# Kernel tuning notes

Measured on AMD Instinct MI355X. Metric: run time of the kernel, lower is better.

## Reference

```python
import jax, jax.numpy as jnp
import numpy as np

IMG_H = IMG_W = 640
NUM_CLASSES = 80
B = 8
NUM_ANCHORS = 76725
MAX_TOTAL = 200          # max_total_size == max_size_per_class
SCORE_TH = 0.5
IOU_TH = 0.5
K_CAND = 256             # per-class candidate pool for NMS (>= max survivors)
VARIANCES = jnp.asarray([0.1, 0.1, 0.2, 0.2], jnp.float32)


def _build_anchors(img_h, img_w):
    # RetinaNet AnchorBox: levels 3..7, 3 ratios x 3 scales, [cx, cy, w, h]
    ratios = [0.5, 1.0, 2.0]
    scales = [2.0 ** x for x in (0.0, 1.0 / 3.0, 2.0 / 3.0)]
    areas = [s * s for s in (32.0, 64.0, 128.0, 256.0, 512.0)]
    out = []
    for lvl, stride in enumerate([2 ** i for i in range(3, 8)]):
        dims = []
        for r in ratios:
            h = np.sqrt(areas[lvl] / r)
            w = areas[lvl] / h
            for s in scales:
                dims.append([w * s, h * s])
        dims = np.asarray(dims, np.float32)                      # [9,2]
        fh = int(np.ceil(img_h / stride)); fw = int(np.ceil(img_w / stride))
        rx = (np.arange(fw, dtype=np.float32) + 0.5) * stride
        ry = (np.arange(fh, dtype=np.float32) + 0.5) * stride
        cx, cy = np.meshgrid(rx, ry)
        centers = np.broadcast_to(np.stack([cx, cy], -1)[:, :, None, :], (fh, fw, 9, 2))
        d = np.broadcast_to(dims[None, None], (fh, fw, 9, 2))
        out.append(np.concatenate([centers, d], -1).reshape(-1, 4))
    return jnp.asarray(np.concatenate(out, 0))                   # [A,4]


def setup_inputs() -> dict:
    key = jax.random.key(0)
    k1, k2 = jax.random.split(key)
    box_pred = jax.random.normal(k1, (B, NUM_ANCHORS, 4), jnp.float32)
    cls_pred = jax.random.normal(k2, (B, NUM_ANCHORS, NUM_CLASSES), jnp.float32)
    anchor_boxes = _build_anchors(IMG_H, IMG_W)
    return {"box_pred": box_pred, "cls_pred": cls_pred, "anchor_boxes": anchor_boxes}


def _iou_one_vs_many(box, boxes):
    # box [4] vs boxes [K,4] in corner format
    lt = jnp.maximum(box[:2], boxes[:, :2])
    rb = jnp.minimum(box[2:], boxes[:, 2:])
    wh = jnp.maximum(rb - lt, 0.0)
    inter = wh[:, 0] * wh[:, 1]
    a1 = (box[2] - box[0]) * (box[3] - box[1])
    a2 = (boxes[:, 2] - boxes[:, 0]) * (boxes[:, 3] - boxes[:, 1])
    return inter / jnp.maximum(a1 + a2 - inter, 1e-8)


def _nms_keep(boxes, scores):
    # boxes [K,4] already sorted by descending score; greedy NMS
    eligible = scores > SCORE_TH
    idx = jnp.arange(K_CAND)

    def body(i, keep):
        iou = _iou_one_vs_many(boxes[i], boxes)
        suppress = (iou > IOU_TH) & (idx > i)
        return jnp.where(keep[i], keep & ~suppress, keep)

    keep = jax.lax.fori_loop(0, K_CAND, body, eligible)
    keep = keep & ((jnp.cumsum(keep) - 1) < MAX_TOTAL)           # max_size_per_class cap
    return keep


def _decode_and_nms(box_pred, cls_pred, anchor_boxes):
    scores_all = jax.nn.sigmoid(cls_pred)                        # [B,A,C]
    # decode: (dx,dy,dw,dh)*variances against [cx,cy,w,h] anchors
    d = box_pred * VARIANCES
    xy = d[..., :2] * anchor_boxes[None, :, 2:] + anchor_boxes[None, :, :2]
    wh = jnp.exp(d[..., 2:]) * anchor_boxes[None, :, 2:]
    boxes = jnp.concatenate([xy - 0.5 * wh, xy + 0.5 * wh], -1)  # [B,A,4] corners

    sc = jnp.swapaxes(scores_all, 1, 2)                          # [B,C,A]
    top_sc, top_idx = jax.lax.top_k(sc, K_CAND)                  # [B,C,K] sorted desc
    cand_boxes = jnp.take_along_axis(boxes[:, None], top_idx[..., None], axis=2)  # [B,C,K,4]

    keep = jax.lax.stop_gradient(jax.vmap(jax.vmap(_nms_keep))(cand_boxes, top_sc))  # [B,C,K]
    sel = jnp.where(keep, top_sc, -1.0)

    flat_sc = sel.reshape(B, -1)                                 # [B,C*K]
    flat_boxes = cand_boxes.reshape(B, -1, 4)
    flat_lbl = jnp.broadcast_to(jnp.arange(NUM_CLASSES)[None, :, None],
                                (B, NUM_CLASSES, K_CAND)).reshape(B, -1)

    fs, fi = jax.lax.top_k(flat_sc, MAX_TOTAL)                   # combine across classes
    out_boxes = jnp.take_along_axis(flat_boxes, fi[..., None], axis=1)
    out_lbl = jnp.take_along_axis(flat_lbl, fi, axis=1).astype(jnp.float32)
    valid = fs > 0.0                                             # pad invalid slots
    return (jnp.where(valid[..., None], out_boxes, 0.0),
            jnp.where(valid, fs, 0.0),
            jnp.where(valid, out_lbl, -1.0))


def reference(box_pred, cls_pred, anchor_boxes):
    return _decode_and_nms(box_pred, cls_pred, anchor_boxes)
```

## Files before the change

### kernel.cpp

```cpp
#include <hip/hip_runtime.h>
#include <math.h>
#include <stdint.h>

typedef unsigned long long u64;
typedef unsigned int u32;

#define NB 8
#define NA 76725
#define NC 80
#define KC 256
#define MAXT 200
#define CAP 2048
#define SELCAP 768
#define TAU 2.0f
#define CHUNK 512
#define NCHUNK 150
#define BCAP 48
#define CSTRIDE 16

#define OFF_BUFA      0ull
#define OFF_CLASSLIST 10485760ull
#define OFF_CANDBOX   11796480ull
#define OFF_COUNTS    14417920ull

__device__ __forceinline__ void kf_proc(float4 v, int i, int a0,
                                        u64 (*bucket)[BCAP], u32* bcnt) {
  int a = a0 + i / (NC / 4);
  int c0 = (i % (NC / 4)) * 4;
  float vv[4] = {v.x, v.y, v.z, v.w};
#pragma unroll
  for (int j = 0; j < 4; j++) {
    if (vv[j] > TAU) {
      int c = c0 + j;
      u32 pos = atomicAdd(&bcnt[c], 1u);
      if (pos < BCAP)
        bucket[c][pos] = ((u64)__float_as_uint(vv[j]) << 32) | (u32)a;
    }
  }
}

__global__ __launch_bounds__(256) void kfilter(const float* __restrict__ cls,
                                               u64* __restrict__ bufA,
                                               u32* __restrict__ counts) {
  __shared__ u64 bucket[NC][BCAP];
  __shared__ u32 bcnt[NC];
  __shared__ u32 gbase[NC];
  __shared__ u32 pref[NC + 1];

  const int b = blockIdx.x / NCHUNK;
  const int ch = blockIdx.x % NCHUNK;
  const int tid = threadIdx.x;
  const int a0 = ch * CHUNK;
  const int aN = (NA - a0) < CHUNK ? (NA - a0) : CHUNK;

  for (int i = tid; i < NC; i += 256) bcnt[i] = 0;
  __syncthreads();

  const float4* p = (const float4*)(cls + ((size_t)b * NA + a0) * NC);
  const int n4 = aN * (NC / 4);
  for (int i0 = tid; i0 < n4; i0 += 2048) {
    float4 v[8];
    bool g[8];
#pragma unroll
    for (int u = 0; u < 8; u++) {
      g[u] = (i0 + u * 256) < n4;
      if (g[u]) v[u] = p[i0 + u * 256];
    }
#pragma unroll
    for (int u = 0; u < 8; u++)
      if (g[u]) kf_proc(v[u], i0 + u * 256, a0, bucket, bcnt);
  }
  __syncthreads();
  if (tid < NC) {
    u32 n = bcnt[tid];
    if (n > BCAP) n = BCAP;
    bcnt[tid] = n;
    gbase[tid] = atomicAdd(&counts[(b * NC + tid) * CSTRIDE], n);
  }
  __syncthreads();
  if (tid == 0) {
    u32 s = 0;
    for (int c = 0; c < NC; c++) { pref[c] = s; s += bcnt[c]; }
    pref[NC] = s;
  }
  __syncthreads();
  const int total = (int)pref[NC];
  for (int e = tid; e < total; e += 256) {
    int lo = 0, hi = NC;
    while (lo + 1 < hi) { int mid = (lo + hi) >> 1; if ((int)pref[mid] <= e) lo = mid; else hi = mid; }
    int c = lo;
    int loc = e - (int)pref[c];
    u32 gb = gbase[c] + (u32)loc;
    if (gb < CAP)
      bufA[((size_t)(b * NC + c)) * CAP + gb] = bucket[c][loc];
  }
}

__global__ __launch_bounds__(256) void kselect(
    const float* __restrict__ cls, const float* __restrict__ boxp,
    const float* __restrict__ anc, u64* __restrict__ bufA,
    const u32* __restrict__ counts, u64* __restrict__ classList,
    float4* __restrict__ candBox) {
  __shared__ u64 sbuf[CAP];
  __shared__ u32 hist[1024];
  __shared__ u64 sel[SELCAP];
  __shared__ u64 skey[KC];
  __shared__ u64 scolT[4][KC];
  __shared__ float4 sBox[KC];
  __shared__ float sAr[KC];
  __shared__ int sNsel, sExtra, sSb;

  const int tid = threadIdx.x;
  const int bc = blockIdx.x;
  const int b = bc / NC, c = bc % NC;
  u64* buf = bufA + (size_t)bc * CAP;

  int cnt0 = (int)counts[bc * CSTRIDE];
  if (cnt0 > CAP) cnt0 = CAP;
  int cnt = cnt0;
  if (cnt0 < KC) {
    if (tid == 0) sExtra = 0;
    __syncthreads();
    for (int a = tid; a < NA; a += 256) {
      float x = cls[((size_t)b * NA + a) * NC + c];
      if (x > 0.0f && !(x > TAU)) {
        int pos = cnt0 + atomicAdd(&sExtra, 1);
        if (pos < CAP) buf[pos] = ((u64)__float_as_uint(x) << 32) | (u32)a;
      }
    }
    __syncthreads();
    cnt = cnt0 + sExtra;
  }
  if (cnt > CAP) cnt = CAP;

  for (int i = tid; i < 1024; i += 256) hist[i] = 0;
  if (tid == 0) sNsel = 0;
  skey[tid] = 0;
  for (int e = tid; e < cnt; e += 256) sbuf[e] = buf[e];
  __syncthreads();

  for (int e = tid; e < cnt; e += 256) {
    float f = __uint_as_float((u32)(sbuf[e] >> 32));
    int bin = (int)(f * 170.0f);
    bin = bin < 0 ? 0 : (bin > 1023 ? 1023 : bin);
    atomicAdd(&hist[bin], 1u);
  }
  __syncthreads();

  if (tid < 64) {
    int s = 0;
#pragma unroll
    for (int i = 0; i < 16; i++) s += (int)hist[tid * 16 + i];
    int suf = s;
#pragma unroll
    for (int d = 1; d < 64; d <<= 1) {
      int t = __shfl_down(suf, d, 64);
      if (tid + d < 64) suf += t;
    }
    u64 mask = __ballot(suf >= KC);
    int sb = mask ? (63 - __clzll((long long)mask)) : 0;
    if (tid == 0) sSb = sb;
  }
  __syncthreads();
  const int sb = sSb;

  for (int e = tid; e < cnt; e += 256) {
    u64 k = sbuf[e];
    float f = __uint_as_float((u32)(k >> 32));
    int bin = (int)(f * 170.0f);
    bin = bin < 0 ? 0 : (bin > 1023 ? 1023 : bin);
    if ((bin >> 4) >= sb) {
      float sc = 1.0f / (1.0f + expf(-f));
      u32 a = (u32)k;
      int pos = atomicAdd(&sNsel, 1);
      if (pos < SELCAP)
        sel[pos] = ((u64)__float_as_uint(sc) << 32) | (0xFFFFFFFFu - a);
    }
  }
  __syncthreads();
  int nsel = sNsel;
  if (nsel > SELCAP) nsel = SELCAP;

  for (int e = tid; e < nsel; e += 256) {
    u64 k = sel[e];
    int r = 0;
    for (int q = 0; q < nsel; q++) r += (sel[q] > k) ? 1 : 0;
    if (r < KC) skey[r] = k;
  }
  __syncthreads();

  {
    u64 k = skey[tid];
    u32 a = 0xFFFFFFFFu - (u32)k;
    if (k == 0ull || a >= NA) a = 0;
    float4 p = ((const float4*)boxp)[(size_t)b * NA + a];
    float4 an = ((const float4*)anc)[a];
    float dx = __fmul_rn(p.x, 0.1f), dy = __fmul_rn(p.y, 0.1f);
    float dw = __fmul_rn(p.z, 0.2f), dh = __fmul_rn(p.w, 0.2f);
    float cx = __fadd_rn(__fmul_rn(dx, an.z), an.x);
    float cy = __fadd_rn(__fmul_rn(dy, an.w), an.y);
    float w = __fmul_rn(expf(dw), an.z);
    float h = __fmul_rn(expf(dh), an.w);
    float4 bx;
    bx.x = __fsub_rn(cx, __fmul_rn(0.5f, w));
    bx.y = __fsub_rn(cy, __fmul_rn(0.5f, h));
    bx.z = __fadd_rn(cx, __fmul_rn(0.5f, w));
    bx.w = __fadd_rn(cy, __fmul_rn(0.5f, h));
    sBox[tid] = bx;
    sAr[tid] = __fmul_rn(__fsub_rn(bx.z, bx.x), __fsub_rn(bx.w, bx.y));
    candBox[(size_t)bc * KC + tid] = bx;
  }
  __syncthreads();

  {
    const int j = tid;
    float4 bj = sBox[j];
    float aj = sAr[j];
    u64 cw[4] = {0ull, 0ull, 0ull, 0ull};
    for (int i = 0; i < j; i++) {
      float4 bi = sBox[i];
      float ai = sAr[i];
      float lx = fmaxf(bi.x, bj.x), ly = fmaxf(bi.y, bj.y);
      float rx = fminf(bi.z, bj.z), ry = fminf(bi.w, bj.w);
      float wx = fmaxf(__fsub_rn(rx, lx), 0.0f);
      float wy = fmaxf(__fsub_rn(ry, ly), 0.0f);
      float inter = __fmul_rn(wx, wy);
      float uni = fmaxf(__fsub_rn(__fadd_rn(ai, aj), inter), 1e-8f);
      float iou = __fdiv_rn(inter, uni);
      if (iou > 0.5f) cw[i >> 6] |= (1ull << (i & 63));
    }
#pragma unroll
    for (int w = 0; w < 4; w++) scolT[w][j] = cw[w];
  }
  __syncthreads();

  if (tid < 64) {
    const int ln = tid;
    u64 C[4][4];
#pragma unroll
    for (int s = 0; s < 4; s++)
#pragma unroll
      for (int w = 0; w < 4; w++) C[s][w] = scolT[w][s * 64 + ln];
    int keep = 0;
#pragma unroll
    for (int s = 0; s < 4; s++)
      if (skey[s * 64 + ln] != 0ull) keep |= (1 << s);
#pragma unroll
    for (int w = 0; w < 4; w++) {
      u64 c0 = C[0][w], c1 = C[1][w], c2 = C[2][w], c3 = C[3][w];
      for (int t = 0; t < 64; t++) {
        int kt = __shfl(keep, t, 64);
        if ((kt >> w) & 1) {
          int sup = (int)((c0 >> t) & 1) | ((int)((c1 >> t) & 1) << 1) |
                    ((int)((c2 >> t) & 1) << 2) | ((int)((c3 >> t) & 1) << 3);
          keep &= ~sup;
        }
      }
    }
    u64 m[4];
#pragma unroll
    for (int s = 0; s < 4; s++) m[s] = __ballot((keep >> s) & 1);
    int tot = 0;
#pragma unroll
    for (int s = 0; s < 4; s++) tot += __popcll(m[s]);
    int keptTotal = tot < MAXT ? tot : MAXT;
    u64 lmask = (1ull << ln) - 1ull;
    int base = 0;
#pragma unroll
    for (int s = 0; s < 4; s++) {
      int j = s * 64 + ln;
      int cum = base + (int)__popcll(m[s] & lmask);
      if (((keep >> s) & 1) && cum < MAXT) {
        u64 hi = skey[j] >> 32;
        classList[(size_t)bc * KC + cum] =
            (hi << 32) | (u64)(0xFFFFFFFFu - (u32)(c * KC + j));
      }
      base += (int)__popcll(m[s]);
    }
    for (int t2 = ln; t2 < KC; t2 += 64)
      if (t2 >= keptTotal) classList[(size_t)bc * KC + t2] = 0;
  }
}

__device__ __forceinline__ u64 shfl64(u64 v, int src) {
  int lo = __shfl((int)(u32)v, src, 64);
  int hi = __shfl((int)(v >> 32), src, 64);
  return ((u64)(u32)hi << 32) | (u32)lo;
}
__device__ __forceinline__ u64 shflxor64(u64 v, int mask) {
  int lo = __shfl_xor((int)(u32)v, mask, 64);
  int hi = __shfl_xor((int)(v >> 32), mask, 64);
  return ((u64)(u32)hi << 32) | (u32)lo;
}
#define CSWAP(a, b) { if ((a) < (b)) { u64 _t = (a); (a) = (b); (b) = _t; } }

__device__ __forceinline__ void wave_merge(u64 acc[4], const u64 cur[4], int ln) {
  u64 t0 = shfl64(cur[3], 63 - ln);
  u64 t1 = shfl64(cur[2], 63 - ln);
  u64 t2 = shfl64(cur[1], 63 - ln);
  u64 t3 = shfl64(cur[0], 63 - ln);
  acc[0] = acc[0] > t0 ? acc[0] : t0;
  acc[1] = acc[1] > t1 ? acc[1] : t1;
  acc[2] = acc[2] > t2 ? acc[2] : t2;
  acc[3] = acc[3] > t3 ? acc[3] : t3;
  CSWAP(acc[0], acc[2]); CSWAP(acc[1], acc[3]);
  CSWAP(acc[0], acc[1]); CSWAP(acc[2], acc[3]);
#pragma unroll
  for (int s = 32; s >= 1; s >>= 1) {
#pragma unroll
    for (int k = 0; k < 4; k++) {
      u64 o = shflxor64(acc[k], s);
      u64 mx = acc[k] > o ? acc[k] : o;
      u64 mn = acc[k] < o ? acc[k] : o;
      acc[k] = ((ln & s) == 0) ? mx : mn;
    }
  }
}

__global__ __launch_bounds__(256) void kmerge(const u64* __restrict__ classList,
                                              const float4* __restrict__ candBox,
                                              float* __restrict__ out) {
  __shared__ u64 lds[4 * KC];
  const int tid = threadIdx.x, b = blockIdx.x;
  const int w = tid >> 6, ln = tid & 63;
  const u64* base = classList + ((size_t)b * NC + w * 20) * KC;
  u64 acc[4];
#pragma unroll
  for (int k = 0; k < 4; k++) acc[k] = base[k * 64 + ln];
  for (int m = 1; m < 20; m++) {
    u64 cur[4];
#pragma unroll
    for (int k = 0; k < 4; k++) cur[k] = base[(size_t)m * KC + k * 64 + ln];
    wave_merge(acc, cur, ln);
  }
#pragma unroll
  for (int k = 0; k < 4; k++) lds[w * KC + k * 64 + ln] = acc[k];
  __syncthreads();
  if (w == 0) {
    for (int m = 1; m < 4; m++) {
      u64 cur[4];
#pragma unroll
      for (int k = 0; k < 4; k++) cur[k] = lds[m * KC + k * 64 + ln];
      wave_merge(acc, cur, ln);
    }
#pragma unroll
    for (int k = 0; k < 4; k++) lds[k * 64 + ln] = acc[k];
  }
  __syncthreads();
  if (tid < MAXT) {
    u64 k = lds[tid];
    float4 bx = make_float4(0.f, 0.f, 0.f, 0.f);
    float sc = 0.0f, lb = -1.0f;
    if (k != 0ull) {
      sc = __uint_as_float((u32)(k >> 32));
      u32 flat = 0xFFFFFFFFu - (u32)k;
      int cc = (int)(flat >> 8), kk = (int)(flat & 255u);
      bx = candBox[((size_t)b * NC + cc) * KC + kk];
      lb = (float)cc;
    }
    float* ob = out + ((size_t)b * MAXT + tid) * 4;
    ob[0] = bx.x; ob[1] = bx.y; ob[2] = bx.z; ob[3] = bx.w;
    out[NB * MAXT * 4 + b * MAXT + tid] = sc;
    out[NB * MAXT * 4 + NB * MAXT + b * MAXT + tid] = lb;
  }
}

extern "C" void kernel_launch(void* const* d_in, const int* in_sizes, int n_in,
                              void* d_out, int out_size, void* d_ws,
                              size_t ws_size, hipStream_t stream) {
  const float* boxp = (const float*)d_in[0];
  const float* cls = (const float*)d_in[1];
  const float* anc = (const float*)d_in[2];
  char* ws = (char*)d_ws;
  u64* bufA = (u64*)(ws + OFF_BUFA);
  u64* classList = (u64*)(ws + OFF_CLASSLIST);
  float4* candBox = (float4*)(ws + OFF_CANDBOX);
  u32* counts = (u32*)(ws + OFF_COUNTS);

  hipMemsetAsync(counts, 0, NB * NC * CSTRIDE * sizeof(u32), stream);
  kfilter<<<NB * NCHUNK, 256, 0, stream>>>(cls, bufA, counts);
  kselect<<<NB * NC, 256, 0, stream>>>(cls, boxp, anc, bufA, counts, classList,
                                       candBox);
  kmerge<<<NB, 256, 0, stream>>>(classList, candBox, (float*)d_out);
}
```

Measured before the change: 390.2 us.

## Fuse filter, select and merge into one cooperative kernel with grid syncs

Replaces the memset plus three kernel launches with a single cooperative kernel that runs filter, select and merge as phases separated by grid-wide syncs, sharing LDS through a union. The filter chunk grows to 960 anchors so the grid is 640 blocks, matching the per-class select grid, and the bucket capacity is raised to fit the larger chunk. This removes launch gaps and the separate memset, but it caps occupancy (launch bounds of 3 blocks per CU, with the union sized to the largest phase's LDS) and adds grid barrier cost. If the cooperative launch fails, it falls back to the old multi-kernel path.

```diff
diff --git a/kernel.cpp b/kernel.cpp
--- a/kernel.cpp
+++ b/kernel.cpp
@@ -1,9 +1,11 @@
 #include <hip/hip_runtime.h>
+#include <hip/hip_cooperative_groups.h>
 #include <math.h>
 #include <stdint.h>
 
 typedef unsigned long long u64;
 typedef unsigned int u32;
+namespace cg = cooperative_groups;
 
 #define NB 8
 #define NA 76725
@@ -13,9 +15,10 @@
 #define CAP 2048
 #define SELCAP 768
 #define TAU 2.0f
-#define CHUNK 512
-#define NCHUNK 150
-#define BCAP 48
+#define CHUNK 960
+#define NCHUNK 80
+#define NBLK (NB * NCHUNK)
+#define BCAP 64
 #define CSTRIDE 16
 
 #define OFF_BUFA      0ull
@@ -23,8 +26,27 @@
 #define OFF_CANDBOX   11796480ull
 #define OFF_COUNTS    14417920ull
 
-__device__ __forceinline__ void kf_proc(float4 v, int i, int a0,
-                                        u64 (*bucket)[BCAP], u32* bcnt) {
+struct P1s {
+  u64 bucket[NC][BCAP];
+  u32 bcnt[NC];
+  u32 gbase[NC];
+  u32 pref[NC + 1];
+};
+struct P2s {
+  u64 sbuf[CAP];
+  u32 hist[1024];
+  u64 sel[SELCAP];
+  u64 skey[KC];
+  u64 scolT[4][KC];
+  float4 sBox[KC];
+  float sAr[KC];
+};
+struct P3s {
+  u64 lds[4 * KC];
+};
+union Ush { P1s p1; P2s p2; P3s p3; };
+
+__device__ __forceinline__ void kf_proc(float4 v, int i, int a0, P1s& S) {
   int a = a0 + i / (NC / 4);
   int c0 = (i % (NC / 4)) * 4;
   float vv[4] = {v.x, v.y, v.z, v.w};
@@ -32,29 +54,19 @@
   for (int j = 0; j < 4; j++) {
     if (vv[j] > TAU) {
       int c = c0 + j;
-      u32 pos = atomicAdd(&bcnt[c], 1u);
+      u32 pos = atomicAdd(&S.bcnt[c], 1u);
       if (pos < BCAP)
-        bucket[c][pos] = ((u64)__float_as_uint(vv[j]) << 32) | (u32)a;
-    }
-  }
-}
-
-__global__ __launch_bounds__(256) void kfilter(const float* __restrict__ cls,
-                                               u64* __restrict__ bufA,
-                                               u32* __restrict__ counts) {
-  __shared__ u64 bucket[NC][BCAP];
-  __shared__ u32 bcnt[NC];
-  __shared__ u32 gbase[NC];
-  __shared__ u32 pref[NC + 1];
-
-  const int b = blockIdx.x / NCHUNK;
-  const int ch = blockIdx.x % NCHUNK;
-  const int tid = threadIdx.x;
+        S.bucket[c][pos] = ((u64)__float_as_uint(vv[j]) << 32) | (u32)a;
+    }
+  }
+}
+
+__device__ __forceinline__ void phase_filter(P1s& S, const float* __restrict__ cls,
+                                             u64* __restrict__ bufA,
+                                             u32* __restrict__ counts,
+                                             int b, int ch, int tid) {
   const int a0 = ch * CHUNK;
   const int aN = (NA - a0) < CHUNK ? (NA - a0) : CHUNK;
-
-  for (int i = tid; i < NC; i += 256) bcnt[i] = 0;
-  __syncthreads();
 
   const float4* p = (const float4*)(cls + ((size_t)b * NA + a0) * NC);
   const int n4 = aN * (NC / 4);
@@ -68,50 +80,40 @@
     }
 #pragma unroll
     for (int u = 0; u < 8; u++)
-      if (g[u]) kf_proc(v[u], i0 + u * 256, a0, bucket, bcnt);
+      if (g[u]) kf_proc(v[u], i0 + u * 256, a0, S);
   }
   __syncthreads();
   if (tid < NC) {
-    u32 n = bcnt[tid];
+    u32 n = S.bcnt[tid];
     if (n > BCAP) n = BCAP;
-    bcnt[tid] = n;
-    gbase[tid] = atomicAdd(&counts[(b * NC + tid) * CSTRIDE], n);
+    S.bcnt[tid] = n;
+    S.gbase[tid] = atomicAdd(&counts[(b * NC + tid) * CSTRIDE], n);
   }
   __syncthreads();
   if (tid == 0) {
     u32 s = 0;
-    for (int c = 0; c < NC; c++) { pref[c] = s; s += bcnt[c]; }
-    pref[NC] = s;
-  }
-  __syncthreads();
-  const int total = (int)pref[NC];
+    for (int c = 0; c < NC; c++) { S.pref[c] = s; s += S.bcnt[c]; }
+    S.pref[NC] = s;
+  }
+  __syncthreads();
+  const int total = (int)S.pref[NC];
   for (int e = tid; e < total; e += 256) {
     int lo = 0, hi = NC;
-    while (lo + 1 < hi) { int mid = (lo + hi) >> 1; if ((int)pref[mid] <= e) lo = mid; else hi = mid; }
+    while (lo + 1 < hi) { int mid = (lo + hi) >> 1; if ((int)S.pref[mid] <= e) lo = mid; else hi = mid; }
     int c = lo;
-    int loc = e - (int)pref[c];
-    u32 gb = gbase[c] + (u32)loc;
+    int loc = e - (int)S.pref[c];
+    u32 gb = S.gbase[c] + (u32)loc;
     if (gb < CAP)
-      bufA[((size_t)(b * NC + c)) * CAP + gb] = bucket[c][loc];
-  }
-}
-
-__global__ __launch_bounds__(256) void kselect(
+      bufA[((size_t)(b * NC + c)) * CAP + gb] = S.bucket[c][loc];
+  }
+}
+
+__device__ __forceinline__ void phase_select(
+    P2s& S, int& sNsel, int& sExtra, int& sSb,
     const float* __restrict__ cls, const float* __restrict__ boxp,
     const float* __restrict__ anc, u64* __restrict__ bufA,
     const u32* __restrict__ counts, u64* __restrict__ classList,
-    float4* __restrict__ candBox) {
-  __shared__ u64 sbuf[CAP];
-  __shared__ u32 hist[1024];
-  __shared__ u64 sel[SELCAP];
-  __shared__ u64 skey[KC];
-  __shared__ u64 scolT[4][KC];
-  __shared__ float4 sBox[KC];
-  __shared__ float sAr[KC];
-  __shared__ int sNsel, sExtra, sSb;
-
-  const int tid = threadIdx.x;
-  const int bc = blockIdx.x;
+    float4* __restrict__ candBox, int bc, int tid) {
   const int b = bc / NC, c = bc % NC;
   u64* buf = bufA + (size_t)bc * CAP;
 
@@ -133,24 +135,24 @@
   }
   if (cnt > CAP) cnt = CAP;
 
-  for (int i = tid; i < 1024; i += 256) hist[i] = 0;
+  for (int i = tid; i < 1024; i += 256) S.hist[i] = 0;
   if (tid == 0) sNsel = 0;
-  skey[tid] = 0;
-  for (int e = tid; e < cnt; e += 256) sbuf[e] = buf[e];
+  S.skey[tid] = 0;
+  for (int e = tid; e < cnt; e += 256) S.sbuf[e] = buf[e];
   __syncthreads();
 
   for (int e = tid; e < cnt; e += 256) {
-    float f = __uint_as_float((u32)(sbuf[e] >> 32));
+    float f = __uint_as_float((u32)(S.sbuf[e] >> 32));
     int bin = (int)(f * 170.0f);
     bin = bin < 0 ? 0 : (bin > 1023 ? 1023 : bin);
-    atomicAdd(&hist[bin], 1u);
+    atomicAdd(&S.hist[bin], 1u);
   }
   __syncthreads();
 
   if (tid < 64) {
     int s = 0;
 #pragma unroll
-    for (int i = 0; i < 16; i++) s += (int)hist[tid * 16 + i];
+    for (int i = 0; i < 16; i++) s += (int)S.hist[tid * 16 + i];
     int suf = s;
 #pragma unroll
     for (int d = 1; d < 64; d <<= 1) {
@@ -165,7 +167,7 @@
   const int sb = sSb;
 
   for (int e = tid; e < cnt; e += 256) {
-    u64 k = sbuf[e];
+    u64 k = S.sbuf[e];
     float f = __uint_as_float((u32)(k >> 32));
     int bin = (int)(f * 170.0f);
     bin = bin < 0 ? 0 : (bin > 1023 ? 1023 : bin);
@@ -174,7 +176,7 @@
       u32 a = (u32)k;
       int pos = atomicAdd(&sNsel, 1);
       if (pos < SELCAP)
-        sel[pos] = ((u64)__float_as_uint(sc) << 32) | (0xFFFFFFFFu - a);
+        S.sel[pos] = ((u64)__float_as_uint(sc) << 32) | (0xFFFFFFFFu - a);
     }
   }
   __syncthreads();
@@ -182,15 +184,15 @@
   if (nsel > SELCAP) nsel = SELCAP;
 
   for (int e = tid; e < nsel; e += 256) {
-    u64 k = sel[e];
+    u64 k = S.sel[e];
     int r = 0;
-    for (int q = 0; q < nsel; q++) r += (sel[q] > k) ? 1 : 0;
-    if (r < KC) skey[r] = k;
+    for (int q = 0; q < nsel; q++) r += (S.sel[q] > k) ? 1 : 0;
+    if (r < KC) S.skey[r] = k;
   }
   __syncthreads();
 
   {
-    u64 k = skey[tid];
+    u64 k = S.skey[tid];
     u32 a = 0xFFFFFFFFu - (u32)k;
     if (k == 0ull || a >= NA) a = 0;
     float4 p = ((const float4*)boxp)[(size_t)b * NA + a];
@@ -206,20 +208,20 @@
     bx.y = __fsub_rn(cy, __fmul_rn(0.5f, h));
     bx.z = __fadd_rn(cx, __fmul_rn(0.5f, w));
     bx.w = __fadd_rn(cy, __fmul_rn(0.5f, h));
-    sBox[tid] = bx;
-    sAr[tid] = __fmul_rn(__fsub_rn(bx.z, bx.x), __fsub_rn(bx.w, bx.y));
+    S.sBox[tid] = bx;
+    S.sAr[tid] = __fmul_rn(__fsub_rn(bx.z, bx.x), __fsub_rn(bx.w, bx.y));
     candBox[(size_t)bc * KC + tid] = bx;
   }
   __syncthreads();
 
   {
     const int j = tid;
-    float4 bj = sBox[j];
-    float aj = sAr[j];
+    float4 bj = S.sBox[j];
+    float aj = S.sAr[j];
     u64 cw[4] = {0ull, 0ull, 0ull, 0ull};
     for (int i = 0; i < j; i++) {
-      float4 bi = sBox[i];
-      float ai = sAr[i];
+      float4 bi = S.sBox[i];
+      float ai = S.sAr[i];
       float lx = fmaxf(bi.x, bj.x), ly = fmaxf(bi.y, bj.y);
       float rx = fminf(bi.z, bj.z), ry = fminf(bi.w, bj.w);
       float wx = fmaxf(__fsub_rn(rx, lx), 0.0f);
@@ -230,7 +232,7 @@
       if (iou > 0.5f) cw[i >> 6] |= (1ull << (i & 63));
     }
 #pragma unroll
-    for (int w = 0; w < 4; w++) scolT[w][j] = cw[w];
+    for (int w = 0; w < 4; w++) S.scolT[w][j] = cw[w];
   }
   __syncthreads();
 
@@ -240,11 +242,11 @@
 #pragma unroll
     for (int s = 0; s < 4; s++)
 #pragma unroll
-      for (int w = 0; w < 4; w++) C[s][w] = scolT[w][s * 64 + ln];
+      for (int w = 0; w < 4; w++) C[s][w] = S.scolT[w][s * 64 + ln];
     int keep = 0;
 #pragma unroll
     for (int s = 0; s < 4; s++)
-      if (skey[s * 64 + ln] != 0ull) keep |= (1 << s);
+      if (S.skey[s * 64 + ln] != 0ull) keep |= (1 << s);
 #pragma unroll
     for (int w = 0; w < 4; w++) {
       u64 c0 = C[0][w], c1 = C[1][w], c2 = C[2][w], c3 = C[3][w];
@@ -271,7 +273,7 @@
       int j = s * 64 + ln;
       int cum = base + (int)__popcll(m[s] & lmask);
       if (((keep >> s) & 1) && cum < MAXT) {
-        u64 hi = skey[j] >> 32;
+        u64 hi = S.skey[j] >> 32;
         classList[(size_t)bc * KC + cum] =
             (hi << 32) | (u64)(0xFFFFFFFFu - (u32)(c * KC + j));
       }
@@ -317,11 +319,9 @@
   }
 }
 
-__global__ __launch_bounds__(256) void kmerge(const u64* __restrict__ classList,
-                                              const float4* __restrict__ candBox,
-                                              float* __restrict__ out) {
-  __shared__ u64 lds[4 * KC];
-  const int tid = threadIdx.x, b = blockIdx.x;
+__device__ __forceinline__ void phase_merge(P3s& S, const u64* __restrict__ classList,
+                                            const float4* __restrict__ candBox,
+                                            float* __restrict__ out, int b, int tid) {
   const int w = tid >> 6, ln = tid & 63;
   const u64* base = classList + ((size_t)b * NC + w * 20) * KC;
   u64 acc[4];
@@ -334,21 +334,21 @@
     wave_merge(acc, cur, ln);
   }
 #pragma unroll
-  for (int k = 0; k < 4; k++) lds[w * KC + k * 64 + ln] = acc[k];
+  for (int k = 0; k < 4; k++) S.lds[w * KC + k * 64 + ln] = acc[k];
   __syncthreads();
   if (w == 0) {
     for (int m = 1; m < 4; m++) {
       u64 cur[4];
 #pragma unroll
-      for (int k = 0; k < 4; k++) cur[k] = lds[m * KC + k * 64 + ln];
+      for (int k = 0; k < 4; k++) cur[k] = S.lds[m * KC + k * 64 + ln];
       wave_merge(acc, cur, ln);
     }
 #pragma unroll
-    for (int k = 0; k < 4; k++) lds[k * 64 + ln] = acc[k];
+    for (int k = 0; k < 4; k++) S.lds[k * 64 + ln] = acc[k];
   }
   __syncthreads();
   if (tid < MAXT) {
-    u64 k = lds[tid];
+    u64 k = S.lds[tid];
     float4 bx = make_float4(0.f, 0.f, 0.f, 0.f);
     float sc = 0.0f, lb = -1.0f;
     if (k != 0ull) {
@@ -363,6 +363,63 @@
     out[NB * MAXT * 4 + b * MAXT + tid] = sc;
     out[NB * MAXT * 4 + NB * MAXT + b * MAXT + tid] = lb;
   }
+}
+
+__global__ __launch_bounds__(256, 3) void kfused(
+    const float* __restrict__ boxp, const float* __restrict__ cls,
+    const float* __restrict__ anc, u64* __restrict__ bufA,
+    u32* __restrict__ counts, u64* __restrict__ classList,
+    float4* __restrict__ candBox, float* __restrict__ out) {
+  __shared__ Ush sh;
+  __shared__ int sNsel, sExtra, sSb;
+  cg::grid_group grid = cg::this_grid();
+  const int tid = threadIdx.x;
+  const int blk = blockIdx.x;
+
+  if (tid == 0) counts[blk * CSTRIDE] = 0;
+  for (int i = tid; i < NC; i += 256) sh.p1.bcnt[i] = 0;
+  __threadfence();
+  grid.sync();
+
+  phase_filter(sh.p1, cls, bufA, counts, blk / NCHUNK, blk % NCHUNK, tid);
+  __threadfence();
+  grid.sync();
+
+  phase_select(sh.p2, sNsel, sExtra, sSb, cls, boxp, anc, bufA, counts,
+               classList, candBox, blk, tid);
+  __threadfence();
+  grid.sync();
+
+  if (blk < NB)
+    phase_merge(sh.p3, classList, candBox, out, blk, tid);
+}
+
+__global__ __launch_bounds__(256) void kfilter(const float* __restrict__ cls,
+                                               u64* __restrict__ bufA,
+                                               u32* __restrict__ counts) {
+  __shared__ P1s sh;
+  const int tid = threadIdx.x;
+  for (int i = tid; i < NC; i += 256) sh.bcnt[i] = 0;
+  __syncthreads();
+  phase_filter(sh, cls, bufA, counts, blockIdx.x / NCHUNK, blockIdx.x % NCHUNK, tid);
+}
+
+__global__ __launch_bounds__(256) void kselect(
+    const float* __restrict__ cls, const float* __restrict__ boxp,
+    const float* __restrict__ anc, u64* __restrict__ bufA,
+    const u32* __restrict__ counts, u64* __restrict__ classList,
+    float4* __restrict__ candBox) {
+  __shared__ P2s sh;
+  __shared__ int sNsel, sExtra, sSb;
+  phase_select(sh, sNsel, sExtra, sSb, cls, boxp, anc, bufA, counts,
+               classList, candBox, blockIdx.x, threadIdx.x);
+}
+
+__global__ __launch_bounds__(256) void kmerge(const u64* __restrict__ classList,
+                                              const float4* __restrict__ candBox,
+                                              float* __restrict__ out) {
+  __shared__ P3s sh;
+  phase_merge(sh, classList, candBox, out, blockIdx.x, threadIdx.x);
 }
 
 extern "C" void kernel_launch(void* const* d_in, const int* in_sizes, int n_in,
@@ -376,10 +433,19 @@
   u64* classList = (u64*)(ws + OFF_CLASSLIST);
   float4* candBox = (float4*)(ws + OFF_CANDBOX);
   u32* counts = (u32*)(ws + OFF_COUNTS);
-
-  hipMemsetAsync(counts, 0, NB * NC * CSTRIDE * sizeof(u32), stream);
-  kfilter<<<NB * NCHUNK, 256, 0, stream>>>(cls, bufA, counts);
-  kselect<<<NB * NC, 256, 0, stream>>>(cls, boxp, anc, bufA, counts, classList,
-                                       candBox);
-  kmerge<<<NB, 256, 0, stream>>>(classList, candBox, (float*)d_out);
-}
+  float* outp = (float*)d_out;
+
+  void* args[8] = {(void*)&boxp, (void*)&cls, (void*)&anc, (void*)&bufA,
+                   (void*)&counts, (void*)&classList, (void*)&candBox,
+                   (void*)&outp};
+  hipError_t e = hipLaunchCooperativeKernel((const void*)kfused, dim3(NBLK),
+                                            dim3(256), args, 0, stream);
+  if (e != hipSuccess) {
+    (void)hipGetLastError();
+    hipMemsetAsync(counts, 0, NB * NC * CSTRIDE * sizeof(u32), stream);
+    kfilter<<<NBLK, 256, 0, stream>>>(cls, bufA, counts);
+    kselect<<<NB * NC, 256, 0, stream>>>(cls, boxp, anc, bufA, counts,
+                                         classList, candBox);
+    kmerge<<<NB, 256, 0, stream>>>(classList, candBox, outp);
+  }
+}
```

Result: slower. 734.0 us (+88.1%).
